# Performance work log

Measured on AMD Instinct MI355X. Metric: run time of the kernel, lower is better.

Reference implementation:

```python
import jax, jax.numpy as jnp
import numpy as np

B, L, C = 2, 2048, 1024
H = 16
HD = C // H  # head_features = 64


def setup_inputs() -> dict:
    key = jax.random.key(0)
    k1, k2, k3, k4, k5, k6 = jax.random.split(key, 6)
    input_x = jax.random.normal(k1, (B, L, C), dtype=jnp.float32)
    x_mask = jax.random.randint(k2, (B, 1, 1, L), 0, 2, dtype=jnp.int32)
    s = 1.0 / np.sqrt(C)
    W_qkv = jax.random.normal(k3, (C, 3 * C), dtype=jnp.float32) * s
    b_qkv = jax.random.normal(k4, (3 * C,), dtype=jnp.float32) * 0.01
    W_proj = jax.random.normal(k5, (C, C), dtype=jnp.float32) * s
    b_proj = jax.random.normal(k6, (C,), dtype=jnp.float32) * 0.01
    return {"input_x": input_x, "x_mask": x_mask, "W_qkv": W_qkv,
            "b_qkv": b_qkv, "W_proj": W_proj, "b_proj": b_proj}


def reference(input_x, x_mask, W_qkv, b_qkv, W_proj, b_proj):
    # qkv projection: [B,L,3C] -> [3,B,H,L,HD]
    qkv = input_x @ W_qkv + b_qkv
    qkv = qkv.reshape(B, L, 3, H, HD).transpose(2, 0, 3, 1, 4)
    q, k, v = qkv[0], qkv[1], qkv[2]
    q = q * (HD ** -0.5)  # first scale (module applies it to q)
    scores = jnp.einsum('bhld,bhmd->bhlm', q, k)  # [B,H,L,L]
    scores = jnp.where(x_mask == 1, jnp.float32(-1e10), scores)
    scores = scores / jnp.sqrt(jnp.float32(HD))  # module's second scale (faithful quirk)
    probs = jax.nn.softmax(scores, axis=-1)
    out = jnp.einsum('bhlm,bhmd->bhld', probs, v)  # [B,H,L,HD]
    out = out.transpose(0, 2, 1, 3).reshape(B, L, C)
    return out @ W_proj + b_proj
```

## Files before the change

kernel.cpp:

```cpp
#include <hip/hip_runtime.h>
#include <stdint.h>

typedef __attribute__((ext_vector_type(8))) short short8;
typedef __attribute__((ext_vector_type(4))) short short4v;
typedef __attribute__((ext_vector_type(4))) float floatx4;
typedef __attribute__((ext_vector_type(16))) float floatx16;

#define B_ 2
#define L_ 2048
#define C_ 1024
#define H_ 16
#define HD_ 64

#define QSCALE (0.015625f * 1.44269504088896f)
#define MASKVAL (-1.8033688e9f)

__device__ __forceinline__ unsigned short f2bf(float f) {
  union { float f; uint32_t u; } v; v.f = f;
  uint32_t r = 0x7FFFu + ((v.u >> 16) & 1u);
  return (unsigned short)((v.u + r) >> 16);
}

__device__ __forceinline__ uint32_t cvtpk(float lo, float hi) {
  uint32_t r;
  asm("v_cvt_pk_bf16_f32 %0, %1, %2" : "=v"(r) : "v"(lo), "v"(hi));
  return r;
}

__device__ __forceinline__ unsigned short f2bf_hw(float f) {
  return (unsigned short)cvtpk(f, f);
}

__device__ __forceinline__ void pl32swap(uint32_t& a, uint32_t& b) {
  asm volatile("v_permlane32_swap_b32 %0, %1" : "+v"(a), "+v"(b));
}

__device__ __forceinline__ void async16(const void* g, void* l) {
  __builtin_amdgcn_global_load_lds(
      (const __attribute__((address_space(1))) void*)g,
      (__attribute__((address_space(3))) void*)l, 16, 0, 0);
}

__global__ __launch_bounds__(256) void cast_bf16_k(const float* __restrict__ in,
                                                   unsigned short* __restrict__ out, int n) {
  int i = (blockIdx.x * 256 + threadIdx.x) * 8;
  if (i >= n) return;
  floatx4 a = *(const floatx4*)(in + i);
  floatx4 b = *(const floatx4*)(in + i + 4);
  short8 o;
  o[0] = (short)f2bf(a[0]); o[1] = (short)f2bf(a[1]);
  o[2] = (short)f2bf(a[2]); o[3] = (short)f2bf(a[3]);
  o[4] = (short)f2bf(b[0]); o[5] = (short)f2bf(b[1]);
  o[6] = (short)f2bf(b[2]); o[7] = (short)f2bf(b[3]);
  *(short8*)(out + i) = o;
}

__global__ __launch_bounds__(256) void transpose_cast_k(const float* __restrict__ in,
                                                        unsigned short* __restrict__ out,
                                                        int R, int Cc) {
  __shared__ float tile[32][33];
  int tx = threadIdx.x, ty = threadIdx.y;
  int c0 = blockIdx.x * 32, r0 = blockIdx.y * 32;
#pragma unroll
  for (int i = 0; i < 4; i++)
    tile[ty + i * 8][tx] = in[(r0 + ty + i * 8) * Cc + c0 + tx];
  __syncthreads();
#pragma unroll
  for (int i = 0; i < 4; i++)
    out[(c0 + ty + i * 8) * R + r0 + tx] = f2bf(tile[tx][ty + i * 8]);
}

__global__ __launch_bounds__(256) void maskpre_k(const int* __restrict__ mask,
                                                 float* __restrict__ maskfg) {
  int i = blockIdx.x * 256 + threadIdx.x;
  if (i < B_ * L_) maskfg[i] = (mask[i] == 1) ? MASKVAL : 0.f;
}

template <int EPI>
__global__ __launch_bounds__(256) void gemm128(const unsigned short* __restrict__ A,
                                               const unsigned short* __restrict__ BT, int K,
                                               int nbx,
                                               const float* __restrict__ bias,
                                               unsigned short* __restrict__ outQ,
                                               unsigned short* __restrict__ outK,
                                               unsigned short* __restrict__ outVT,
                                               float* __restrict__ outF) {
  __shared__ __attribute__((aligned(16))) unsigned short Asmem[2][128 * 32];
  __shared__ __attribute__((aligned(16))) unsigned short Bsmem[2][128 * 32];
  const int t = threadIdx.x;
  const int wave = t >> 6, lane = t & 63;
  const int wr = wave >> 1, wc = wave & 1;
  const int nwg = gridDim.x;
  const int id = (blockIdx.x & 7) * (nwg >> 3) + (blockIdx.x >> 3);
  const int bx = id % nbx, by = id / nbx;
  const int row0 = by * 128, col0 = bx * 128;

  const int arow = row0 + (t >> 2), brow = col0 + (t >> 2);
  const int koff = (t & 3) * 8;

#define STAGE(buf, k0)                                                               \
  {                                                                                  \
    async16(A + (size_t)arow * K + (k0) + koff, &Asmem[buf][t * 8]);                 \
    async16(A + (size_t)(arow + 64) * K + (k0) + koff, &Asmem[buf][(256 + t) * 8]);  \
    async16(BT + (size_t)brow * K + (k0) + koff, &Bsmem[buf][t * 8]);                \
    async16(BT + (size_t)(brow + 64) * K + (k0) + koff, &Bsmem[buf][(256 + t) * 8]); \
  }

  floatx4 acc[4][4] = {};
  STAGE(0, 0);
  __syncthreads();
  int cur = 0;
  for (int k0 = 0; k0 < K; k0 += 32) {
    if (k0 + 32 < K) STAGE(cur ^ 1, k0 + 32);
    short8 af[4], bfr[4];
#pragma unroll
    for (int m = 0; m < 4; m++)
      af[m] = *(const short8*)(&Asmem[cur][(wr * 64 + m * 16 + (lane & 15)) * 32 +
                                           (lane >> 4) * 8]);
#pragma unroll
    for (int n = 0; n < 4; n++)
      bfr[n] = *(const short8*)(&Bsmem[cur][(wc * 64 + n * 16 + (lane & 15)) * 32 +
                                            (lane >> 4) * 8]);
#pragma unroll
    for (int m = 0; m < 4; m++)
#pragma unroll
      for (int n = 0; n < 4; n++)
        acc[m][n] = __builtin_amdgcn_mfma_f32_16x16x32_bf16(af[m], bfr[n], acc[m][n], 0, 0, 0);
    __syncthreads();
    cur ^= 1;
  }
#undef STAGE

#pragma unroll
  for (int m = 0; m < 4; m++)
#pragma unroll
    for (int n = 0; n < 4; n++) {
      const int r0e = row0 + wr * 64 + m * 16 + (lane >> 4) * 4;
      const int cc = col0 + wc * 64 + n * 16 + (lane & 15);
      const float bv = bias[cc];
      if (EPI == 2) {
#pragma unroll
        for (int j = 0; j < 4; j++)
          outF[(size_t)(r0e + j) * C_ + cc] = acc[m][n][j] + bv;
      } else {
        const int which = col0 >> 10;
        const int rem = cc & 1023, h = rem >> 6, d = rem & 63;
        const int bb = r0e >> 11, l0 = r0e & 2047;
        const size_t base = (size_t)(bb * H_ + h) * (L_ * HD_);
        if (which == 0) {
#pragma unroll
          for (int j = 0; j < 4; j++)
            outQ[base + (size_t)(l0 + j) * HD_ + d] = f2bf_hw((acc[m][n][j] + bv) * QSCALE);
        } else if (which == 1) {
          const size_t kbase =
              base + ((l0 >> 5) * 8 + (d >> 4) * 2 + ((d >> 3) & 1)) * 256 + (d & 7);
#pragma unroll
          for (int j = 0; j < 4; j++)
            outK[kbase + ((l0 & 31) + j) * 8] = f2bf_hw(acc[m][n][j] + bv);
        } else {
          const size_t vbase = base +
                               ((((l0 >> 7) * 2 + (d >> 5)) * 8 + ((l0 >> 4) & 7)) * 2 +
                                ((l0 >> 3) & 1)) * 256 +
                               (d & 31) * 8 + (l0 & 7);
          union { unsigned short s[4]; short4v v; } ov;
#pragma unroll
          for (int j = 0; j < 4; j++) ov.s[j] = f2bf_hw(acc[m][n][j] + bv);
          *(short4v*)(outVT + vbase) = ov.v;
        }
      }
    }
}

__global__ __launch_bounds__(256) void attn_k(const unsigned short* __restrict__ Q,
                                              const unsigned short* __restrict__ Kf,
                                              const unsigned short* __restrict__ VTf,
                                              const float* __restrict__ maskfg,
                                              unsigned short* __restrict__ attn_out) {
  __shared__ __attribute__((aligned(16))) unsigned short Ks[128 * 64];
  __shared__ __attribute__((aligned(16))) unsigned short VTs[64 * 128];
  __shared__ __attribute__((aligned(16))) float maskL[L_];

  const int t = threadIdx.x, wave = t >> 6, lane = t & 63;
  const int h = lane >> 5, c32 = lane & 31;
  const int bh = blockIdx.x & 31;
  const int qt = blockIdx.x >> 5;
  const int b = bh >> 4, hh = bh & 15;
  const unsigned short* Qp = Q + (size_t)bh * L_ * HD_;
  const unsigned short* Kp = Kf + (size_t)bh * L_ * HD_;
  const unsigned short* VTp = VTf + (size_t)bh * L_ * HD_;
  const int qrow = qt * 128 + wave * 32 + c32;

  short8 qf[4];
#pragma unroll
  for (int ks = 0; ks < 4; ks++)
    qf[ks] = *(const short8*)(Qp + (size_t)qrow * HD_ + ks * 16 + h * 8);

#pragma unroll
  for (int i = 0; i < 2; i++) {
    int idx = i * 256 + t;
    async16(maskfg + b * L_ + idx * 4, maskL + idx * 4);
  }

  floatx16 o[2] = {};
  float lrun = 0.f;

  for (int kv = 0; kv < 16; kv++) {
    __syncthreads();
#pragma unroll
    for (int i = 0; i < 4; i++) {
      int idx = i * 256 + t;
      async16(Kp + (size_t)kv * 8192 + idx * 8, Ks + idx * 8);
    }
#pragma unroll
    for (int i = 0; i < 4; i++) {
      int idx = i * 256 + t;
      async16(VTp + (size_t)kv * 8192 + idx * 8, VTs + idx * 8);
    }
    __syncthreads();

    floatx16 s[4];
#pragma unroll
    for (int kg = 0; kg < 4; kg++) {
#pragma unroll
      for (int rr = 0; rr < 4; rr++) {
        floatx4 mk = *(const floatx4*)(maskL + kv * 128 + kg * 32 + rr * 8 + h * 4);
#pragma unroll
        for (int jj = 0; jj < 4; jj++) s[kg][rr * 4 + jj] = mk[jj];
      }
#pragma unroll
      for (int ks = 0; ks < 4; ks++) {
        const short8 kfr = *(const short8*)(Ks + ((kg * 4 + ks) * 2 + h) * 256 + c32 * 8);
        s[kg] = __builtin_amdgcn_mfma_f32_32x32x16_bf16(kfr, qf[ks], s[kg], 0, 0, 0);
      }
    }

    float rs = 0.f;
#pragma unroll
    for (int kg = 0; kg < 4; kg++)
#pragma unroll
      for (int e = 0; e < 16; e++) {
        float p = __builtin_amdgcn_exp2f(s[kg][e]);
        s[kg][e] = p;
        rs += p;
      }
    rs += __shfl_xor(rs, 32);
    lrun += rs;

#pragma unroll
    for (int kg = 0; kg < 4; kg++) {
      uint32_t pk[8];
#pragma unroll
      for (int e = 0; e < 8; e++) pk[e] = cvtpk(s[kg][2 * e], s[kg][2 * e + 1]);
#pragma unroll
      for (int ts = 0; ts < 2; ts++) {
        uint32_t x0 = pk[4 * ts + 0], x1 = pk[4 * ts + 1];
        uint32_t y0 = pk[4 * ts + 2], y1 = pk[4 * ts + 3];
        pl32swap(x0, y0);
        pl32swap(x1, y1);
        union { uint32_t u[4]; short8 v; } pf;
        pf.u[0] = x0; pf.u[1] = x1; pf.u[2] = y0; pf.u[3] = y1;
        const int kt = kg * 2 + ts;
#pragma unroll
        for (int dg = 0; dg < 2; dg++) {
          const short8 vfr = *(const short8*)(VTs + ((dg * 8 + kt) * 2 + h) * 256 + c32 * 8);
          o[dg] = __builtin_amdgcn_mfma_f32_32x32x16_bf16(vfr, pf.v, o[dg], 0, 0, 0);
        }
      }
    }
  }

  const float inv = 1.f / lrun;
#pragma unroll
  for (int dg = 0; dg < 2; dg++)
#pragma unroll
    for (int rr = 0; rr < 4; rr++) {
      short4v ov;
#pragma unroll
      for (int jj = 0; jj < 4; jj++) ov[jj] = (short)f2bf(o[dg][rr * 4 + jj] * inv);
      int d0 = dg * 32 + rr * 8 + h * 4;
      *(short4v*)(attn_out + ((size_t)b * L_ + qrow) * C_ + hh * HD_ + d0) = ov;
    }
}

extern "C" void kernel_launch(void* const* d_in, const int* in_sizes, int n_in,
                              void* d_out, int out_size, void* d_ws, size_t ws_size,
                              hipStream_t stream) {
  const float* x = (const float*)d_in[0];
  const int* mask = (const int*)d_in[1];
  const float* Wqkv = (const float*)d_in[2];
  const float* bqkv = (const float*)d_in[3];
  const float* Wproj = (const float*)d_in[4];
  const float* bproj = (const float*)d_in[5];
  float* out = (float*)d_out;
  char* ws = (char*)d_ws;

  unsigned short* Xb = (unsigned short*)(ws);
  unsigned short* WqkvT = (unsigned short*)(ws + (8u << 20));
  unsigned short* WprojT = (unsigned short*)(ws + (14u << 20));
  unsigned short* Qb = (unsigned short*)(ws + (16u << 20));
  unsigned short* Kb = (unsigned short*)(ws + (24u << 20));
  unsigned short* VTb = (unsigned short*)(ws + (32u << 20));
  unsigned short* AOb = Xb;
  float* maskfg = (float*)(ws + (8u << 20));

  cast_bf16_k<<<(B_ * L_ * C_) / 8 / 256, 256, 0, stream>>>(x, Xb, B_ * L_ * C_);
  dim3 tb(32, 8);
  transpose_cast_k<<<dim3(3 * C_ / 32, C_ / 32), tb, 0, stream>>>(Wqkv, WqkvT, C_, 3 * C_);
  transpose_cast_k<<<dim3(C_ / 32, C_ / 32), tb, 0, stream>>>(Wproj, WprojT, C_, C_);

  gemm128<1><<<768, 256, 0, stream>>>(Xb, WqkvT, C_, 24, bqkv, Qb, Kb, VTb, nullptr);

  maskpre_k<<<(B_ * L_) / 256, 256, 0, stream>>>(mask, maskfg);

  attn_k<<<B_ * H_ * (L_ / 128), 256, 0, stream>>>(Qb, Kb, VTb, maskfg, AOb);

  gemm128<2><<<256, 256, 0, stream>>>(AOb, WprojT, C_, 8, bproj, nullptr, nullptr, nullptr, out);
}
```

Measured before the change: 121.4 us.

## Double-buffer K/V tiles in LDS to overlap loads with attention compute

Splits the K and V^T shared-memory tiles into two buffers and prefetches the next KV tile while the current one is computed. Explicit vmcnt waits and barriers replace the two syncthreads per iteration, so global load latency can be hidden behind MFMA and exp work. It doubles LDS use for K/V, which can lower the number of resident blocks per CU.

```diff
diff --git a/kernel.cpp b/kernel.cpp
--- a/kernel.cpp
+++ b/kernel.cpp
@@ -176,8 +176,10 @@
                                               const unsigned short* __restrict__ VTf,
                                               const float* __restrict__ maskfg,
                                               unsigned short* __restrict__ attn_out) {
-  __shared__ __attribute__((aligned(16))) unsigned short Ks[128 * 64];
-  __shared__ __attribute__((aligned(16))) unsigned short VTs[64 * 128];
+  __shared__ __attribute__((aligned(16))) unsigned short Ks0[128 * 64];
+  __shared__ __attribute__((aligned(16))) unsigned short VTs0[64 * 128];
+  __shared__ __attribute__((aligned(16))) unsigned short Ks1[128 * 64];
+  __shared__ __attribute__((aligned(16))) unsigned short VTs1[64 * 128];
   __shared__ __attribute__((aligned(16))) float maskL[L_];
 
   const int t = threadIdx.x, wave = t >> 6, lane = t & 63;
@@ -195,79 +197,94 @@
   for (int ks = 0; ks < 4; ks++)
     qf[ks] = *(const short8*)(Qp + (size_t)qrow * HD_ + ks * 16 + h * 8);
 
+#define STAGEKV(KSB, VTB, kv)                                            \
+  {                                                                      \
+    _Pragma("unroll") for (int i = 0; i < 4; i++) {                      \
+      int idx = i * 256 + t;                                             \
+      async16(Kp + (size_t)(kv)*8192 + idx * 8, KSB + idx * 8);          \
+    }                                                                    \
+    _Pragma("unroll") for (int i = 0; i < 4; i++) {                      \
+      int idx = i * 256 + t;                                             \
+      async16(VTp + (size_t)(kv)*8192 + idx * 8, VTB + idx * 8);         \
+    }                                                                    \
+  }
+
+  floatx16 o[2] = {};
+  float lrun = 0.f;
+
+#define COMPUTE(KSB, VTB, kv)                                                          \
+  {                                                                                    \
+    floatx16 s[4];                                                                     \
+    _Pragma("unroll") for (int kg = 0; kg < 4; kg++) {                                 \
+      _Pragma("unroll") for (int rr = 0; rr < 4; rr++) {                               \
+        floatx4 mk = *(const floatx4*)(maskL + (kv)*128 + kg * 32 + rr * 8 + h * 4);   \
+        _Pragma("unroll") for (int jj = 0; jj < 4; jj++) s[kg][rr * 4 + jj] = mk[jj];  \
+      }                                                                                \
+      _Pragma("unroll") for (int ks = 0; ks < 4; ks++) {                               \
+        const short8 kfr = *(const short8*)(KSB + ((kg * 4 + ks) * 2 + h) * 256 + c32 * 8); \
+        s[kg] = __builtin_amdgcn_mfma_f32_32x32x16_bf16(kfr, qf[ks], s[kg], 0, 0, 0);  \
+      }                                                                                \
+    }                                                                                  \
+    float rs = 0.f;                                                                    \
+    _Pragma("unroll") for (int kg = 0; kg < 4; kg++)                                   \
+        _Pragma("unroll") for (int e = 0; e < 16; e++) {                               \
+      float p = __builtin_amdgcn_exp2f(s[kg][e]);                                      \
+      s[kg][e] = p;                                                                    \
+      rs += p;                                                                         \
+    }                                                                                  \
+    rs += __shfl_xor(rs, 32);                                                          \
+    lrun += rs;                                                                        \
+    _Pragma("unroll") for (int kg = 0; kg < 4; kg++) {                                 \
+      uint32_t pk[8];                                                                  \
+      _Pragma("unroll") for (int e = 0; e < 8; e++)                                    \
+          pk[e] = cvtpk(s[kg][2 * e], s[kg][2 * e + 1]);                               \
+      _Pragma("unroll") for (int ts = 0; ts < 2; ts++) {                               \
+        uint32_t x0 = pk[4 * ts + 0], x1 = pk[4 * ts + 1];                             \
+        uint32_t y0 = pk[4 * ts + 2], y1 = pk[4 * ts + 3];                             \
+        pl32swap(x0, y0);                                                              \
+        pl32swap(x1, y1);                                                              \
+        union { uint32_t u[4]; short8 v; } pf;                                         \
+        pf.u[0] = x0; pf.u[1] = x1; pf.u[2] = y0; pf.u[3] = y1;                        \
+        const int kt = kg * 2 + ts;                                                    \
+        _Pragma("unroll") for (int dg = 0; dg < 2; dg++) {                             \
+          const short8 vfr =                                                           \
+              *(const short8*)(VTB + ((dg * 8 + kt) * 2 + h) * 256 + c32 * 8);         \
+          o[dg] = __builtin_amdgcn_mfma_f32_32x32x16_bf16(vfr, pf.v, o[dg], 0, 0, 0);  \
+        }                                                                              \
+      }                                                                                \
+    }                                                                                  \
+  }
+
+#define PHASE(KC, VC, KN, VN, kv, nkv)                         \
+  {                                                            \
+    if ((nkv) < 16) {                                          \
+      STAGEKV(KN, VN, nkv);                                    \
+      asm volatile("s_waitcnt vmcnt(8)" ::: "memory");         \
+    } else {                                                   \
+      asm volatile("s_waitcnt vmcnt(0)" ::: "memory");         \
+    }                                                          \
+    __builtin_amdgcn_sched_barrier(0);                         \
+    __builtin_amdgcn_s_barrier();                              \
+    __builtin_amdgcn_sched_barrier(0);                         \
+    COMPUTE(KC, VC, kv);                                       \
+    __builtin_amdgcn_s_barrier();                              \
+  }
+
 #pragma unroll
   for (int i = 0; i < 2; i++) {
     int idx = i * 256 + t;
     async16(maskfg + b * L_ + idx * 4, maskL + idx * 4);
   }
-
-  floatx16 o[2] = {};
-  float lrun = 0.f;
-
-  for (int kv = 0; kv < 16; kv++) {
-    __syncthreads();
-#pragma unroll
-    for (int i = 0; i < 4; i++) {
-      int idx = i * 256 + t;
-      async16(Kp + (size_t)kv * 8192 + idx * 8, Ks + idx * 8);
-    }
-#pragma unroll
-    for (int i = 0; i < 4; i++) {
-      int idx = i * 256 + t;
-      async16(VTp + (size_t)kv * 8192 + idx * 8, VTs + idx * 8);
-    }
-    __syncthreads();
-
-    floatx16 s[4];
-#pragma unroll
-    for (int kg = 0; kg < 4; kg++) {
-#pragma unroll
-      for (int rr = 0; rr < 4; rr++) {
-        floatx4 mk = *(const floatx4*)(maskL + kv * 128 + kg * 32 + rr * 8 + h * 4);
-#pragma unroll
-        for (int jj = 0; jj < 4; jj++) s[kg][rr * 4 + jj] = mk[jj];
-      }
-#pragma unroll
-      for (int ks = 0; ks < 4; ks++) {
-        const short8 kfr = *(const short8*)(Ks + ((kg * 4 + ks) * 2 + h) * 256 + c32 * 8);
-        s[kg] = __builtin_amdgcn_mfma_f32_32x32x16_bf16(kfr, qf[ks], s[kg], 0, 0, 0);
-      }
-    }
-
-    float rs = 0.f;
-#pragma unroll
-    for (int kg = 0; kg < 4; kg++)
-#pragma unroll
-      for (int e = 0; e < 16; e++) {
-        float p = __builtin_amdgcn_exp2f(s[kg][e]);
-        s[kg][e] = p;
-        rs += p;
-      }
-    rs += __shfl_xor(rs, 32);
-    lrun += rs;
-
-#pragma unroll
-    for (int kg = 0; kg < 4; kg++) {
-      uint32_t pk[8];
-#pragma unroll
-      for (int e = 0; e < 8; e++) pk[e] = cvtpk(s[kg][2 * e], s[kg][2 * e + 1]);
-#pragma unroll
-      for (int ts = 0; ts < 2; ts++) {
-        uint32_t x0 = pk[4 * ts + 0], x1 = pk[4 * ts + 1];
-        uint32_t y0 = pk[4 * ts + 2], y1 = pk[4 * ts + 3];
-        pl32swap(x0, y0);
-        pl32swap(x1, y1);
-        union { uint32_t u[4]; short8 v; } pf;
-        pf.u[0] = x0; pf.u[1] = x1; pf.u[2] = y0; pf.u[3] = y1;
-        const int kt = kg * 2 + ts;
-#pragma unroll
-        for (int dg = 0; dg < 2; dg++) {
-          const short8 vfr = *(const short8*)(VTs + ((dg * 8 + kt) * 2 + h) * 256 + c32 * 8);
-          o[dg] = __builtin_amdgcn_mfma_f32_32x32x16_bf16(vfr, pf.v, o[dg], 0, 0, 0);
-        }
-      }
-    }
-  }
+  STAGEKV(Ks0, VTs0, 0);
+
+#pragma unroll 1
+  for (int kv2 = 0; kv2 < 16; kv2 += 2) {
+    PHASE(Ks0, VTs0, Ks1, VTs1, kv2, kv2 + 1);
+    PHASE(Ks1, VTs1, Ks0, VTs0, kv2 + 1, kv2 + 2);
+  }
+#undef PHASE
+#undef COMPUTE
+#undef STAGEKV
 
   const float inv = 1.f / lrun;
 #pragma unroll
```

After: 122.6 us. Within noise of the previous version (+1.0%).

## Inject mask via rank-1 MFMA, use bf16 mask, narrow proj GEMM tile

Applied to the files above, without the earlier changes.

The attention kernel now stores the mask as bf16 in shared memory. It seeds each score accumulator with an outer-product MFMA (mask column times a one-hot vector) instead of loading 16 floats per group into registers. This aims to cut LDS traffic and register pressure. The exp/row-sum loop is split into four independent accumulators to shorten the dependency chain. The output-projection GEMM switches to 128x64 tiles with 512 blocks to improve CU occupancy for that small GEMM, at the cost of more A re-reads. Rounding the mask value to bf16 shifts it slightly, which should still underflow exp2 to zero.

```diff
diff --git a/kernel.cpp b/kernel.cpp
--- a/kernel.cpp
+++ b/kernel.cpp
@@ -71,12 +71,12 @@
 }
 
 __global__ __launch_bounds__(256) void maskpre_k(const int* __restrict__ mask,
-                                                 float* __restrict__ maskfg) {
+                                                 unsigned short* __restrict__ maskbf) {
   int i = blockIdx.x * 256 + threadIdx.x;
-  if (i < B_ * L_) maskfg[i] = (mask[i] == 1) ? MASKVAL : 0.f;
-}
-
-template <int EPI>
+  if (i < B_ * L_) maskbf[i] = (mask[i] == 1) ? f2bf(MASKVAL) : (unsigned short)0;
+}
+
+template <int EPI, int BN>
 __global__ __launch_bounds__(256) void gemm128(const unsigned short* __restrict__ A,
                                                const unsigned short* __restrict__ BT, int K,
                                                int nbx,
@@ -86,45 +86,48 @@
                                                unsigned short* __restrict__ outVT,
                                                float* __restrict__ outF) {
   __shared__ __attribute__((aligned(16))) unsigned short Asmem[2][128 * 32];
-  __shared__ __attribute__((aligned(16))) unsigned short Bsmem[2][128 * 32];
+  __shared__ __attribute__((aligned(16))) unsigned short Bsmem[2][BN * 32];
   const int t = threadIdx.x;
   const int wave = t >> 6, lane = t & 63;
   const int wr = wave >> 1, wc = wave & 1;
+  const int NW = BN / 2;
+  const int NF = BN / 32;
   const int nwg = gridDim.x;
   const int id = (blockIdx.x & 7) * (nwg >> 3) + (blockIdx.x >> 3);
   const int bx = id % nbx, by = id / nbx;
-  const int row0 = by * 128, col0 = bx * 128;
+  const int row0 = by * 128, col0 = bx * BN;
 
   const int arow = row0 + (t >> 2), brow = col0 + (t >> 2);
   const int koff = (t & 3) * 8;
 
-#define STAGE(buf, k0)                                                               \
-  {                                                                                  \
-    async16(A + (size_t)arow * K + (k0) + koff, &Asmem[buf][t * 8]);                 \
-    async16(A + (size_t)(arow + 64) * K + (k0) + koff, &Asmem[buf][(256 + t) * 8]);  \
-    async16(BT + (size_t)brow * K + (k0) + koff, &Bsmem[buf][t * 8]);                \
-    async16(BT + (size_t)(brow + 64) * K + (k0) + koff, &Bsmem[buf][(256 + t) * 8]); \
+#define STAGE(buf, k0)                                                                 \
+  {                                                                                    \
+    async16(A + (size_t)arow * K + (k0) + koff, &Asmem[buf][t * 8]);                   \
+    async16(A + (size_t)(arow + 64) * K + (k0) + koff, &Asmem[buf][(256 + t) * 8]);    \
+    async16(BT + (size_t)brow * K + (k0) + koff, &Bsmem[buf][t * 8]);                  \
+    if (BN == 128)                                                                     \
+      async16(BT + (size_t)(brow + 64) * K + (k0) + koff, &Bsmem[buf][(256 + t) * 8]); \
   }
 
-  floatx4 acc[4][4] = {};
+  floatx4 acc[4][NF] = {};
   STAGE(0, 0);
   __syncthreads();
   int cur = 0;
   for (int k0 = 0; k0 < K; k0 += 32) {
     if (k0 + 32 < K) STAGE(cur ^ 1, k0 + 32);
-    short8 af[4], bfr[4];
+    short8 af[4], bfr[NF];
 #pragma unroll
     for (int m = 0; m < 4; m++)
       af[m] = *(const short8*)(&Asmem[cur][(wr * 64 + m * 16 + (lane & 15)) * 32 +
                                            (lane >> 4) * 8]);
 #pragma unroll
-    for (int n = 0; n < 4; n++)
-      bfr[n] = *(const short8*)(&Bsmem[cur][(wc * 64 + n * 16 + (lane & 15)) * 32 +
+    for (int n = 0; n < NF; n++)
+      bfr[n] = *(const short8*)(&Bsmem[cur][(wc * NW + n * 16 + (lane & 15)) * 32 +
                                             (lane >> 4) * 8]);
 #pragma unroll
     for (int m = 0; m < 4; m++)
 #pragma unroll
-      for (int n = 0; n < 4; n++)
+      for (int n = 0; n < NF; n++)
         acc[m][n] = __builtin_amdgcn_mfma_f32_16x16x32_bf16(af[m], bfr[n], acc[m][n], 0, 0, 0);
     __syncthreads();
     cur ^= 1;
@@ -134,9 +137,9 @@
 #pragma unroll
   for (int m = 0; m < 4; m++)
 #pragma unroll
-    for (int n = 0; n < 4; n++) {
+    for (int n = 0; n < NF; n++) {
       const int r0e = row0 + wr * 64 + m * 16 + (lane >> 4) * 4;
-      const int cc = col0 + wc * 64 + n * 16 + (lane & 15);
+      const int cc = col0 + wc * NW + n * 16 + (lane & 15);
       const float bv = bias[cc];
       if (EPI == 2) {
 #pragma unroll
@@ -174,11 +177,11 @@
 __global__ __launch_bounds__(256) void attn_k(const unsigned short* __restrict__ Q,
                                               const unsigned short* __restrict__ Kf,
                                               const unsigned short* __restrict__ VTf,
-                                              const float* __restrict__ maskfg,
+                                              const unsigned short* __restrict__ maskbf,
                                               unsigned short* __restrict__ attn_out) {
   __shared__ __attribute__((aligned(16))) unsigned short Ks[128 * 64];
   __shared__ __attribute__((aligned(16))) unsigned short VTs[64 * 128];
-  __shared__ __attribute__((aligned(16))) float maskL[L_];
+  __shared__ __attribute__((aligned(16))) unsigned short maskLb[L_];
 
   const int t = threadIdx.x, wave = t >> 6, lane = t & 63;
   const int h = lane >> 5, c32 = lane & 31;
@@ -195,11 +198,14 @@
   for (int ks = 0; ks < 4; ks++)
     qf[ks] = *(const short8*)(Qp + (size_t)qrow * HD_ + ks * 16 + h * 8);
 
-#pragma unroll
-  for (int i = 0; i < 2; i++) {
-    int idx = i * 256 + t;
-    async16(maskfg + b * L_ + idx * 4, maskL + idx * 4);
-  }
+  union { uint32_t u[4]; short8 v; } onef;
+  onef.u[0] = h ? 0u : 0x3F80u;
+  onef.u[1] = 0; onef.u[2] = 0; onef.u[3] = 0;
+  floatx16 z16;
+#pragma unroll
+  for (int e = 0; e < 16; e++) z16[e] = 0.f;
+
+  async16(maskbf + b * L_ + t * 8, maskLb + t * 8);
 
   floatx16 o[2] = {};
   float lrun = 0.f;
@@ -221,12 +227,11 @@
     floatx16 s[4];
 #pragma unroll
     for (int kg = 0; kg < 4; kg++) {
-#pragma unroll
-      for (int rr = 0; rr < 4; rr++) {
-        floatx4 mk = *(const floatx4*)(maskL + kv * 128 + kg * 32 + rr * 8 + h * 4);
-#pragma unroll
-        for (int jj = 0; jj < 4; jj++) s[kg][rr * 4 + jj] = mk[jj];
-      }
+      union { uint32_t u[4]; short8 v; } mf;
+      unsigned short mval = maskLb[kv * 128 + kg * 32 + c32];
+      mf.u[0] = h ? 0u : (uint32_t)mval;
+      mf.u[1] = 0; mf.u[2] = 0; mf.u[3] = 0;
+      s[kg] = __builtin_amdgcn_mfma_f32_32x32x16_bf16(mf.v, onef.v, z16, 0, 0, 0);
 #pragma unroll
       for (int ks = 0; ks < 4; ks++) {
         const short8 kfr = *(const short8*)(Ks + ((kg * 4 + ks) * 2 + h) * 256 + c32 * 8);
@@ -234,15 +239,20 @@
       }
     }
 
-    float rs = 0.f;
+    float r0 = 0.f, r1 = 0.f, r2 = 0.f, r3 = 0.f;
 #pragma unroll
     for (int kg = 0; kg < 4; kg++)
 #pragma unroll
-      for (int e = 0; e < 16; e++) {
-        float p = __builtin_amdgcn_exp2f(s[kg][e]);
-        s[kg][e] = p;
-        rs += p;
+      for (int q = 0; q < 4; q++) {
+        float p0 = __builtin_amdgcn_exp2f(s[kg][4 * q + 0]);
+        float p1 = __builtin_amdgcn_exp2f(s[kg][4 * q + 1]);
+        float p2 = __builtin_amdgcn_exp2f(s[kg][4 * q + 2]);
+        float p3 = __builtin_amdgcn_exp2f(s[kg][4 * q + 3]);
+        s[kg][4 * q + 0] = p0; s[kg][4 * q + 1] = p1;
+        s[kg][4 * q + 2] = p2; s[kg][4 * q + 3] = p3;
+        r0 += p0; r1 += p1; r2 += p2; r3 += p3;
       }
+    float rs = (r0 + r1) + (r2 + r3);
     rs += __shfl_xor(rs, 32);
     lrun += rs;
 
@@ -262,7 +272,8 @@
         const int kt = kg * 2 + ts;
 #pragma unroll
         for (int dg = 0; dg < 2; dg++) {
-          const short8 vfr = *(const short8*)(VTs + ((dg * 8 + kt) * 2 + h) * 256 + c32 * 8);
+          const short8 vfr =
+              *(const short8*)(VTs + ((dg * 8 + kt) * 2 + h) * 256 + c32 * 8);
           o[dg] = __builtin_amdgcn_mfma_f32_32x32x16_bf16(vfr, pf.v, o[dg], 0, 0, 0);
         }
       }
@@ -301,18 +312,19 @@
   unsigned short* Kb = (unsigned short*)(ws + (24u << 20));
   unsigned short* VTb = (unsigned short*)(ws + (32u << 20));
   unsigned short* AOb = Xb;
-  float* maskfg = (float*)(ws + (8u << 20));
+  unsigned short* maskbf = (unsigned short*)(ws + (8u << 20));
 
   cast_bf16_k<<<(B_ * L_ * C_) / 8 / 256, 256, 0, stream>>>(x, Xb, B_ * L_ * C_);
   dim3 tb(32, 8);
   transpose_cast_k<<<dim3(3 * C_ / 32, C_ / 32), tb, 0, stream>>>(Wqkv, WqkvT, C_, 3 * C_);
   transpose_cast_k<<<dim3(C_ / 32, C_ / 32), tb, 0, stream>>>(Wproj, WprojT, C_, C_);
 
-  gemm128<1><<<768, 256, 0, stream>>>(Xb, WqkvT, C_, 24, bqkv, Qb, Kb, VTb, nullptr);
-
-  maskpre_k<<<(B_ * L_) / 256, 256, 0, stream>>>(mask, maskfg);
-
-  attn_k<<<B_ * H_ * (L_ / 128), 256, 0, stream>>>(Qb, Kb, VTb, maskfg, AOb);
-
-  gemm128<2><<<256, 256, 0, stream>>>(AOb, WprojT, C_, 8, bproj, nullptr, nullptr, nullptr, out);
-}
+  gemm128<1, 128><<<768, 256, 0, stream>>>(Xb, WqkvT, C_, 24, bqkv, Qb, Kb, VTb, nullptr);
+
+  maskpre_k<<<(B_ * L_) / 256, 256, 0, stream>>>(mask, maskbf);
+
+  attn_k<<<B_ * H_ * (L_ / 128), 256, 0, stream>>>(Qb, Kb, VTb, maskbf, AOb);
+
+  gemm128<2, 64><<<512, 256, 0, stream>>>(AOb, WprojT, C_, 16, bproj, nullptr, nullptr, nullptr,
+                                          out);
+}
```

After: 118.1 us. -2.8%, faster.
